# Optimization experiments

Measured on AMD Instinct MI355X. Metric: run time of the kernel, lower is better.

The kernel has to match this reference:

```python
import jax, jax.numpy as jnp
import numpy as np

S, B, D, H, L = 512, 512, 300, 256, 3

def setup_inputs() -> dict:
    key = jax.random.key(0)
    ks = jax.random.split(key, 9)
    sc = 0.02
    return {
        "x": jax.random.normal(ks[0], (S, B, D), dtype=jnp.float32),
        "fW_ih0": jax.random.normal(ks[1], (D, H), dtype=jnp.float32) * sc,
        "fW_ih": jax.random.normal(ks[2], (L - 1, H, H), dtype=jnp.float32) * sc,
        "fW_hh": jax.random.normal(ks[3], (L, H, H), dtype=jnp.float32) * sc,
        "fb": jnp.zeros((L, H), dtype=jnp.float32),
        "bW_ih0": jax.random.normal(ks[4], (D, H), dtype=jnp.float32) * sc,
        "bW_ih": jax.random.normal(ks[5], (L - 1, H, H), dtype=jnp.float32) * sc,
        "bW_hh": jax.random.normal(ks[6], (L, H, H), dtype=jnp.float32) * sc,
        "bb": jnp.zeros((L, H), dtype=jnp.float32),
    }

def _run_rnn(x, W_ih0, W_ih, W_hh, b):
    # x: [S, B, D]; stacked vanilla tanh RNN with L layers.
    batch = x.shape[1]
    h0 = jnp.zeros((L, batch, H), dtype=x.dtype)

    def step(h, x_t):  # h: [L, B, H], x_t: [B, D]
        inp = x_t
        new_h = []
        for l in range(L):
            Wih = W_ih0 if l == 0 else W_ih[l - 1]
            hl = jnp.tanh(inp @ Wih + h[l] @ W_hh[l] + b[l])
            new_h.append(hl)
            inp = hl
        return jnp.stack(new_h, axis=0), None

    h_final, _ = jax.lax.scan(step, h0, x)
    return h_final  # [L, B, H]

def reference(x, fW_ih0, fW_ih, fW_hh, fb, bW_ih0, bW_ih, bW_hh, bb):
    hf = _run_rnn(x, fW_ih0, fW_ih, fW_hh, fb)          # forward direction
    hb = _run_rnn(x[::-1], bW_ih0, bW_ih, bW_hh, bb)    # backward direction
    return jnp.concatenate((hf[-1], hb[-1]), axis=-1)   # [B, 2H]
```

## Files before the change

### kernel.cpp

```cpp
#include <hip/hip_runtime.h>
#include <cstdint>
#include <cstddef>


#define SEQ   512
#define BATCH 512
#define DIN   300
#define HDIM  256
#define NT    512
#define CH    64
#define NCH   (SEQ / CH)
#define NSLOT (NCH + 2)
#define TS    16
#define ZTILE 131072

typedef _Float16 f16x8 __attribute__((ext_vector_type(8)));
typedef __fp16   fp16x2 __attribute__((ext_vector_type(2)));
typedef float    f32x4 __attribute__((ext_vector_type(4)));

#define WIH0_E 0
#define WHH_E  163840
#define WIHN_E 557056
#define HC_BYTE   1638400
#define HB_BYTE   3211264
#define Z0_BYTE   (HB_BYTE + 67108864)
#define Z1_BYTE   (Z0_BYTE + 268435456)
#define Z2_BYTE   (Z1_BYTE + 67108864)
#define RING_E    8388608ull

static __device__ __forceinline__ uint16_t f16bits(_Float16 h) {
    union { _Float16 h; uint16_t u; } v; v.h = h; return v.u;
}
static __device__ __forceinline__ uint32_t pk2(float a, float b) {
    union { fp16x2 h; uint32_t u; } v; v.h = __builtin_amdgcn_cvt_pkrtz(a, b); return v.u;
}
static __device__ __forceinline__ int swz(int row, int col) {
    return (row * 256 + col) ^ ((row & 7) << 3);
}

static __device__ __forceinline__ void aload8(f16x8 r[8], const _Float16* p, size_t stepE) {
    const _Float16* p0 = p;
    const _Float16* p1 = p + stepE;
    const _Float16* p2 = p + 2 * stepE;
    const _Float16* p3 = p + 3 * stepE;
    const _Float16* p4 = p + 4 * stepE;
    const _Float16* p5 = p + 5 * stepE;
    const _Float16* p6 = p + 6 * stepE;
    const _Float16* p7 = p + 7 * stepE;
    asm volatile(
        "global_load_dwordx4 %0, %8, off\n\t"
        "global_load_dwordx4 %1, %9, off\n\t"
        "global_load_dwordx4 %2, %10, off\n\t"
        "global_load_dwordx4 %3, %11, off\n\t"
        "global_load_dwordx4 %4, %12, off\n\t"
        "global_load_dwordx4 %5, %13, off\n\t"
        "global_load_dwordx4 %6, %14, off\n\t"
        "global_load_dwordx4 %7, %15, off\n\t"
        "s_waitcnt vmcnt(0)"
        : "=&v"(r[0]), "=&v"(r[1]), "=&v"(r[2]), "=&v"(r[3]),
          "=&v"(r[4]), "=&v"(r[5]), "=&v"(r[6]), "=&v"(r[7])
        : "v"(p0), "v"(p1), "v"(p2), "v"(p3), "v"(p4), "v"(p5), "v"(p6), "v"(p7)
        : "memory");
}

__global__ void rnn_prep(const float* __restrict__ fW_ih0, const float* __restrict__ fW_ih,
                         const float* __restrict__ fW_hh,  const float* __restrict__ bW_ih0,
                         const float* __restrict__ bW_ih,  const float* __restrict__ bW_hh,
                         _Float16* __restrict__ wf)
{
    const int gid = blockIdx.x * 256 + threadIdx.x;
    const int d = gid / 51200;
    const int r = gid - d * 51200;
    const int lane = r & 63;
    const float* Wih0 = d ? bW_ih0 : fW_ih0;
    const float* Wih  = d ? bW_ih  : fW_ih;
    const float* Whh  = d ? bW_hh  : fW_hh;
    _Float16 vals[8];
    size_t dstE;
    if (r < 10240) {
        const int ck = r >> 6, ct = ck / 10, kt = ck - ct * 10;
        const int col = ct * 16 + (lane & 15);
        const int k0  = kt * 32 + (lane >> 4) * 8;
        #pragma unroll
        for (int e = 0; e < 8; ++e) {
            const int k = k0 + e;
            vals[e] = (k < 300) ? (_Float16)Wih0[(size_t)k * 256 + col] : (_Float16)0.f;
        }
        dstE = (size_t)WIH0_E + (size_t)d * 81920 + (size_t)r * 8;
    } else if (r < 34816) {
        const int rr = r - 10240, l = rr / 8192, r2 = rr - l * 8192;
        const int ck = r2 >> 6, ct = ck >> 3, kt = ck & 7;
        const int col = ct * 16 + (lane & 15);
        const int k0  = kt * 32 + (lane >> 4) * 8;
        #pragma unroll
        for (int e = 0; e < 8; ++e)
            vals[e] = (_Float16)Whh[((size_t)(l * 256 + k0 + e)) * 256 + col];
        dstE = (size_t)WHH_E + (size_t)(d * 3 + l) * 65536 + (size_t)r2 * 8;
    } else {
        const int rr = r - 34816, ln = rr / 8192, r2 = rr - ln * 8192;
        const int ck = r2 >> 6, ct = ck >> 3, kt = ck & 7;
        const int col = ct * 16 + (lane & 15);
        const int k0  = kt * 32 + (lane >> 4) * 8;
        #pragma unroll
        for (int e = 0; e < 8; ++e)
            vals[e] = (_Float16)Wih[((size_t)(ln * 256 + k0 + e)) * 256 + col];
        dstE = (size_t)WIHN_E + (size_t)(d * 2 + ln) * 65536 + (size_t)r2 * 8;
    }
    *(f16x8*)(wf + dstE) = *(const f16x8*)vals;
}

__global__ __attribute__((amdgpu_flat_work_group_size(NT, NT)))
void rnn_gemm0(const float* __restrict__ x, const _Float16* __restrict__ wih0,
               const float* __restrict__ fb, const float* __restrict__ bb,
               uint16_t* __restrict__ z0)
{
    __shared__ uint16_t Xl[2][16 * 332];
    const int tid = threadIdx.x, lane = tid & 63, w = tid >> 6;
    const int colw = lane & 15, rq = lane >> 4, rq8 = rq * 8;
    const int ct0 = w * 2;
    const int sg = blockIdx.x >> 5, rb = blockIdx.x & 31;
    const int b0 = rb * 16;
    const size_t chunk = ((size_t)(rb * 8 + w) * 64 + lane) * 8;

    int rs[5], cc2[5]; bool pv[5];
    #pragma unroll
    for (int b = 0; b < 5; ++b) {
        const int p = tid + b * NT;
        pv[b] = p < 2400;
        const int r = p / 150;
        rs[b] = r; cc2[b] = (p - r * 150) * 2;
    }

    float bv[2][2];
    #pragma unroll
    for (int dd = 0; dd < 2; ++dd)
        #pragma unroll
        for (int c = 0; c < 2; ++c)
            bv[dd][c] = (dd ? bb : fb)[(ct0 + c) * 16 + colw];

    for (int p = tid; p < 320; p += NT) {
        const int bu = p / 160, q = p - bu * 160;
        const int r = q / 10, cc = 300 + (q - r * 10) * 2;
        *(uint32_t*)&Xl[bu][r * 332 + cc] = 0;
    }
    {
        const float* xs = x + ((size_t)(sg * TS) * BATCH + b0) * DIN;
        #pragma unroll
        for (int b = 0; b < 5; ++b) if (pv[b]) {
            const float2 v = *(const float2*)(xs + (size_t)rs[b] * DIN + cc2[b]);
            *(uint32_t*)&Xl[0][rs[b] * 332 + cc2[b]] = pk2(v.x, v.y);
        }
    }
    __syncthreads();

    #pragma unroll 1
    for (int si = 0; si < TS; ++si) {
        const int s = sg * TS + si;
        const int buf = si & 1;
        const bool last = (si == TS - 1);

        {
            f32x4 a0 = (f32x4){bv[0][0], bv[0][0], bv[0][0], bv[0][0]};
            f32x4 a1 = (f32x4){bv[0][1], bv[0][1], bv[0][1], bv[0][1]};
            #pragma unroll
            for (int kt = 0; kt < 10; ++kt) {
                const f16x8 wv0 = *(const f16x8*)(wih0 + (((size_t)ct0 * 10 + kt) * 64 + lane) * 8);
                const f16x8 wv1 = *(const f16x8*)(wih0 + (((size_t)(ct0 + 1) * 10 + kt) * 64 + lane) * 8);
                const f16x8 a = *(const f16x8*)&Xl[buf][colw * 332 + kt * 32 + rq8];
                a0 = __builtin_amdgcn_mfma_f32_16x16x32_f16(a, wv0, a0, 0, 0, 0);
                a1 = __builtin_amdgcn_mfma_f32_16x16x32_f16(a, wv1, a1, 0, 0, 0);
            }
            uint4 sv;
            sv.x = pk2(a0[0], a0[1]); sv.y = pk2(a0[2], a0[3]);
            sv.z = pk2(a1[0], a1[1]); sv.w = pk2(a1[2], a1[3]);
            *(uint4*)(z0 + (size_t)s * ZTILE + chunk) = sv;
        }

        float2 xr[5];
        if (!last) {
            const float* xs = x + ((size_t)(s + 1) * BATCH + b0) * DIN;
            #pragma unroll
            for (int b = 0; b < 5; ++b) if (pv[b])
                xr[b] = *(const float2*)(xs + (size_t)rs[b] * DIN + cc2[b]);
        }

        f32x4 a0 = (f32x4){bv[1][0], bv[1][0], bv[1][0], bv[1][0]};
        f32x4 a1 = (f32x4){bv[1][1], bv[1][1], bv[1][1], bv[1][1]};
        #pragma unroll
        for (int kt = 0; kt < 10; ++kt) {
            const f16x8 wv0 = *(const f16x8*)(wih0 + 81920 + (((size_t)ct0 * 10 + kt) * 64 + lane) * 8);
            const f16x8 wv1 = *(const f16x8*)(wih0 + 81920 + (((size_t)(ct0 + 1) * 10 + kt) * 64 + lane) * 8);
            const f16x8 a = *(const f16x8*)&Xl[buf][colw * 332 + kt * 32 + rq8];
            a0 = __builtin_amdgcn_mfma_f32_16x16x32_f16(a, wv0, a0, 0, 0, 0);
            a1 = __builtin_amdgcn_mfma_f32_16x16x32_f16(a, wv1, a1, 0, 0, 0);
        }

        if (!last) {
            #pragma unroll
            for (int b = 0; b < 5; ++b) if (pv[b])
                *(uint32_t*)&Xl[buf ^ 1][rs[b] * 332 + cc2[b]] = pk2(xr[b].x, xr[b].y);
        }

        {
            uint4 sv;
            sv.x = pk2(a0[0], a0[1]); sv.y = pk2(a0[2], a0[3]);
            sv.z = pk2(a1[0], a1[1]); sv.w = pk2(a1[2], a1[3]);
            *(uint4*)(z0 + ((size_t)SEQ + (SEQ - 1 - s)) * ZTILE + chunk) = sv;
        }

        __builtin_amdgcn_sched_barrier(0);
        asm volatile("s_waitcnt lgkmcnt(0)" ::: "memory");
        __builtin_amdgcn_s_barrier();
        __builtin_amdgcn_sched_barrier(0);
    }
}

template<int L>
__device__ __forceinline__ void rec_run(const _Float16* whh_all, const _Float16* wihn_all,
                                        const uint16_t* zsrc, uint16_t* zdst,
                                        uint16_t* hcarry, const float* fb, const float* bb,
                                        float* out, int d, int i, int cs, uint16_t* Hb)
{
    const int tid = threadIdx.x, lane = tid & 63, w = tid >> 6;
    const int colw = lane & 15, rq = lane >> 4, rq8 = rq * 8;
    const int ct0 = w * 2;
    const int grow0 = i * 16;

    const _Float16* whh = whh_all + (size_t)(d * 3 + L) * 65536;
    f16x8 wh0[8], wh1[8];
    aload8(wh0, whh + ((size_t)ct0 * 8 * 64 + lane) * 8, 512);
    aload8(wh1, whh + ((size_t)(ct0 + 1) * 8 * 64 + lane) * 8, 512);
    f16x8 wn0[8], wn1[8];
    float bn0 = 0.f, bn1 = 0.f;
    if constexpr (L < 2) {
        const _Float16* wnx = wihn_all + (size_t)(d * 2 + L) * 65536;
        aload8(wn0, wnx + ((size_t)ct0 * 8 * 64 + lane) * 8, 512);
        aload8(wn1, wnx + ((size_t)(ct0 + 1) * 8 * 64 + lane) * 8, 512);
        const float* bnx = (d ? bb : fb) + (L + 1) * HDIM;
        bn0 = bnx[ct0 * 16 + colw];
        bn1 = bnx[(ct0 + 1) * 16 + colw];
    }

    for (int p = tid; p < 4096; p += NT) ((uint32_t*)Hb)[p] = 0;
    __syncthreads();
    if (cs > 0) {
        const uint16_t* hc = hcarry + (size_t)(d * 3 + L) * 131072;
        const int row = tid >> 5, c8 = (tid & 31) * 8;
        *(uint4*)&Hb[4096 + ((row * 256 + c8) ^ ((row & 7) << 3))] =
            *(const uint4*)(hc + (size_t)(grow0 + row) * 256 + c8);
    }
    __syncthreads();

    const size_t zoff = ((size_t)(i * 8 + w) * 64 + lane) * 8;

    uint4 zc = *(const uint4*)(zsrc + zoff);
    uint4 za = *(const uint4*)(zsrc + (size_t)ZTILE + zoff);
    uint4 zb = *(const uint4*)(zsrc + 2 * (size_t)ZTILE + zoff);

    f32x4 anp0 = {}, anp1 = {};

    #pragma unroll 1
    for (int k = 0; k < CH; ++k) {
        const int cur = k & 1, prv = cur ^ 1;
        const int kp = (k + 3 < CH) ? (k + 3) : (CH - 1);
        const uint4 zd = *(const uint4*)(zsrc + (size_t)kp * ZTILE + zoff);

        f16x8 ah[8];
        #pragma unroll
        for (int kt = 0; kt < 8; ++kt)
            ah[kt] = *(const f16x8*)&Hb[(prv << 12) + swz(colw, kt * 32 + rq8)];

        f32x4 ar0, ar1;
        {
            union { uint4 u; _Float16 h[8]; } zz; zz.u = zc;
            ar0 = (f32x4){(float)zz.h[0], (float)zz.h[1], (float)zz.h[2], (float)zz.h[3]};
            ar1 = (f32x4){(float)zz.h[4], (float)zz.h[5], (float)zz.h[6], (float)zz.h[7]};
        }

        f32x4 an0, an1;
        if constexpr (L < 2) {
            an0 = (f32x4){bn0, bn0, bn0, bn0};
            an1 = (f32x4){bn1, bn1, bn1, bn1};
            #pragma unroll
            for (int kt = 0; kt < 8; ++kt) {
                ar0 = __builtin_amdgcn_mfma_f32_16x16x32_f16(ah[kt], wh0[kt], ar0, 0, 0, 0);
                ar1 = __builtin_amdgcn_mfma_f32_16x16x32_f16(ah[kt], wh1[kt], ar1, 0, 0, 0);
                an0 = __builtin_amdgcn_mfma_f32_16x16x32_f16(ah[kt], wn0[kt], an0, 0, 0, 0);
                an1 = __builtin_amdgcn_mfma_f32_16x16x32_f16(ah[kt], wn1[kt], an1, 0, 0, 0);
            }
        } else {
            f32x4 arB0 = {}, arB1 = {};
            #pragma unroll
            for (int kt = 0; kt < 4; ++kt) {
                ar0  = __builtin_amdgcn_mfma_f32_16x16x32_f16(ah[kt],     wh0[kt],     ar0,  0, 0, 0);
                ar1  = __builtin_amdgcn_mfma_f32_16x16x32_f16(ah[kt],     wh1[kt],     ar1,  0, 0, 0);
                arB0 = __builtin_amdgcn_mfma_f32_16x16x32_f16(ah[4 + kt], wh0[4 + kt], arB0, 0, 0, 0);
                arB1 = __builtin_amdgcn_mfma_f32_16x16x32_f16(ah[4 + kt], wh1[4 + kt], arB1, 0, 0, 0);
            }
            ar0 = ar0 + arB0;
            ar1 = ar1 + arB1;
        }

        if constexpr (L < 2) {
            if (k >= 2) {
                uint4 sv;
                sv.x = pk2(anp0[0], anp0[1]); sv.y = pk2(anp0[2], anp0[3]);
                sv.z = pk2(anp1[0], anp1[1]); sv.w = pk2(anp1[2], anp1[3]);
                *(uint4*)(zdst + (size_t)(k - 2) * ZTILE + zoff) = sv;
            }
        }

        float hv[8];
        #pragma unroll
        for (int q = 0; q < 8; ++q) {
            const float S = (q < 4) ? ar0[q] : ar1[q - 4];
            const float e = __builtin_amdgcn_exp2f(S * 2.885390081777927f);
            const float r = __builtin_amdgcn_rcpf(e + 1.f);
            hv[q] = __builtin_fmaf(-2.f, r, 1.f);
        }
        #pragma unroll
        for (int q = 0; q < 8; ++q) {
            const int c = q >> 2, j = q & 3;
            Hb[(cur << 12) + swz(rq * 4 + j, (ct0 + c) * 16 + colw)] = f16bits((_Float16)hv[q]);
        }
        if (L == 2 && cs == NCH - 1 && k == CH - 1) {
            #pragma unroll
            for (int q = 0; q < 8; ++q) {
                const int c = q >> 2, j = q & 3;
                out[(size_t)(grow0 + rq * 4 + j) * 512 + d * 256 + (ct0 + c) * 16 + colw] = hv[q];
            }
        }

        if constexpr (L < 2) { anp0 = an0; anp1 = an1; }
        zc = za; za = zb; zb = zd;

        __builtin_amdgcn_sched_barrier(0);
        asm volatile("s_waitcnt lgkmcnt(0)" ::: "memory");
        __builtin_amdgcn_s_barrier();
        __builtin_amdgcn_sched_barrier(0);
    }

    if constexpr (L < 2) {
        {
            uint4 sv;
            sv.x = pk2(anp0[0], anp0[1]); sv.y = pk2(anp0[2], anp0[3]);
            sv.z = pk2(anp1[0], anp1[1]); sv.w = pk2(anp1[2], anp1[3]);
            *(uint4*)(zdst + (size_t)(CH - 2) * ZTILE + zoff) = sv;
        }
        f32x4 an0 = (f32x4){bn0, bn0, bn0, bn0};
        f32x4 an1 = (f32x4){bn1, bn1, bn1, bn1};
        #pragma unroll
        for (int kt = 0; kt < 8; ++kt) {
            const f16x8 ah = *(const f16x8*)&Hb[(1 << 12) + swz(colw, kt * 32 + rq8)];
            an0 = __builtin_amdgcn_mfma_f32_16x16x32_f16(ah, wn0[kt], an0, 0, 0, 0);
            an1 = __builtin_amdgcn_mfma_f32_16x16x32_f16(ah, wn1[kt], an1, 0, 0, 0);
        }
        uint4 sv;
        sv.x = pk2(an0[0], an0[1]); sv.y = pk2(an0[2], an0[3]);
        sv.z = pk2(an1[0], an1[1]); sv.w = pk2(an1[2], an1[3]);
        *(uint4*)(zdst + (size_t)(CH - 1) * ZTILE + zoff) = sv;
    }
    {
        uint16_t* hc = hcarry + (size_t)(d * 3 + L) * 131072;
        const int row = tid >> 5, c8 = (tid & 31) * 8;
        *(uint4*)(hc + (size_t)(grow0 + row) * 256 + c8) =
            *(const uint4*)&Hb[4096 + ((row * 256 + c8) ^ ((row & 7) << 3))];
    }
}

__global__ __attribute__((amdgpu_flat_work_group_size(NT, NT), amdgpu_waves_per_eu(2)))
void rnn_rec(const _Float16* whh_all, const _Float16* wihn_all,
             uint16_t* z0, uint16_t* z1, uint16_t* z2,
             uint16_t* hcarry, const float* fb, const float* bb,
             float* out, int slot)
{
    __shared__ uint16_t Hb[2 * 4096];
    const int l = blockIdx.x >> 6, sub = blockIdx.x & 63;
    const int d = sub >> 5, i = sub & 31;
    const int cs = slot - l;
    if (cs < 0 || cs >= NCH) return;
    const size_t ringE = (size_t)((cs & 1) * 2 + d) * RING_E;
    if (l == 0) {
        const uint16_t* zs = z0 + ((size_t)d * SEQ + (size_t)cs * CH) * ZTILE;
        rec_run<0>(whh_all, wihn_all, zs, z1 + ringE, hcarry, fb, bb, out, d, i, cs, Hb);
    } else if (l == 1) {
        rec_run<1>(whh_all, wihn_all, z1 + ringE, z2 + ringE, hcarry, fb, bb, out, d, i, cs, Hb);
    } else {
        rec_run<2>(whh_all, wihn_all, z2 + ringE, nullptr, hcarry, fb, bb, out, d, i, cs, Hb);
    }
}

extern "C" void kernel_launch(void* const* d_in, const int* in_sizes, int n_in,
                              void* d_out, int out_size, void* d_ws, size_t ws_size,
                              hipStream_t stream)
{
    (void)in_sizes; (void)n_in; (void)out_size; (void)ws_size;
    const float* x      = (const float*)d_in[0];
    const float* fW_ih0 = (const float*)d_in[1];
    const float* fW_ih  = (const float*)d_in[2];
    const float* fW_hh  = (const float*)d_in[3];
    const float* fb     = (const float*)d_in[4];
    const float* bW_ih0 = (const float*)d_in[5];
    const float* bW_ih  = (const float*)d_in[6];
    const float* bW_hh  = (const float*)d_in[7];
    const float* bb     = (const float*)d_in[8];
    uint8_t* ws = (uint8_t*)d_ws;

    _Float16* wf     = (_Float16*)ws;
    uint16_t* hcarry = (uint16_t*)(ws + HC_BYTE);
    uint16_t* z0     = (uint16_t*)(ws + Z0_BYTE);
    uint16_t* z1     = (uint16_t*)(ws + Z1_BYTE);
    uint16_t* z2     = (uint16_t*)(ws + Z2_BYTE);
    const _Float16* whh  = wf + WHH_E;
    const _Float16* wihn = wf + WIHN_E;
    float* out = (float*)d_out;

    rnn_prep<<<400, 256, 0, stream>>>(fW_ih0, fW_ih, fW_hh, bW_ih0, bW_ih, bW_hh, wf);
    rnn_gemm0<<<1024, NT, 0, stream>>>(x, wf, fb, bb, z0);
    for (int s = 0; s < NSLOT; ++s)
        rnn_rec<<<192, NT, 0, stream>>>(whh, wihn, z0, z1, z2, hcarry, fb, bb, out, s);
}
```

Before: 872.9 us.

## Fuse input GEMM into slot kernel and overlap with recurrence chunks

The standalone input-projection GEMM is removed. Each slot launch now runs, next to the recurrent blocks, 128 extra blocks that compute the layer-0 input projections for the following chunk, so that GEMM overlaps the latency-bound recurrence. The recurrent loop is unrolled by four with a four-deep register prefetch ring for z, and the layer-0 MFMA chains are split into two accumulators. Weight loads no longer wait inside the asm helper; a separate drain waits for them. This adds one launch, shares LDS between the two roles, and raises register pressure.

Result: slower. 991.4 us (+13.6%).

```diff
diff --git a/kernel.cpp b/kernel.cpp
--- a/kernel.cpp
+++ b/kernel.cpp
@@ -10,9 +10,9 @@
 #define NT    512
 #define CH    64
 #define NCH   (SEQ / CH)
-#define NSLOT (NCH + 2)
 #define TS    16
 #define ZTILE 131072
+#define XLBUF 5312
 
 typedef _Float16 f16x8 __attribute__((ext_vector_type(8)));
 typedef __fp16   fp16x2 __attribute__((ext_vector_type(2)));
@@ -55,12 +55,15 @@
         "global_load_dwordx4 %4, %12, off\n\t"
         "global_load_dwordx4 %5, %13, off\n\t"
         "global_load_dwordx4 %6, %14, off\n\t"
-        "global_load_dwordx4 %7, %15, off\n\t"
-        "s_waitcnt vmcnt(0)"
+        "global_load_dwordx4 %7, %15, off"
         : "=&v"(r[0]), "=&v"(r[1]), "=&v"(r[2]), "=&v"(r[3]),
           "=&v"(r[4]), "=&v"(r[5]), "=&v"(r[6]), "=&v"(r[7])
         : "v"(p0), "v"(p1), "v"(p2), "v"(p3), "v"(p4), "v"(p5), "v"(p6), "v"(p7)
         : "memory");
+}
+static __device__ __forceinline__ void adrain() {
+    asm volatile("s_waitcnt vmcnt(0)" ::: "memory");
+    __builtin_amdgcn_sched_barrier(0);
 }
 
 __global__ void rnn_prep(const float* __restrict__ fW_ih0, const float* __restrict__ fW_ih,
@@ -109,18 +112,20 @@
     *(f16x8*)(wf + dstE) = *(const f16x8*)vals;
 }
 
-__global__ __attribute__((amdgpu_flat_work_group_size(NT, NT)))
-void rnn_gemm0(const float* __restrict__ x, const _Float16* __restrict__ wih0,
-               const float* __restrict__ fb, const float* __restrict__ bb,
-               uint16_t* __restrict__ z0)
+__device__ __forceinline__ void gemm0_chunk(const float* __restrict__ x,
+                                            const _Float16* __restrict__ wih0,
+                                            const float* __restrict__ fb,
+                                            const float* __restrict__ bb,
+                                            uint16_t* __restrict__ z0,
+                                            int chunk, int gb, uint16_t* Xl)
 {
-    __shared__ uint16_t Xl[2][16 * 332];
     const int tid = threadIdx.x, lane = tid & 63, w = tid >> 6;
     const int colw = lane & 15, rq = lane >> 4, rq8 = rq * 8;
     const int ct0 = w * 2;
-    const int sg = blockIdx.x >> 5, rb = blockIdx.x & 31;
+    const int sg4 = gb >> 5, rb = gb & 31;
     const int b0 = rb * 16;
-    const size_t chunk = ((size_t)(rb * 8 + w) * 64 + lane) * 8;
+    const int sbase = chunk * CH + sg4 * TS;
+    const size_t chunkoff = ((size_t)(rb * 8 + w) * 64 + lane) * 8;
 
     int rs[5], cc2[5]; bool pv[5];
     #pragma unroll
@@ -141,21 +146,21 @@
     for (int p = tid; p < 320; p += NT) {
         const int bu = p / 160, q = p - bu * 160;
         const int r = q / 10, cc = 300 + (q - r * 10) * 2;
-        *(uint32_t*)&Xl[bu][r * 332 + cc] = 0;
+        *(uint32_t*)&Xl[bu * XLBUF + r * 332 + cc] = 0;
     }
     {
-        const float* xs = x + ((size_t)(sg * TS) * BATCH + b0) * DIN;
+        const float* xs = x + ((size_t)sbase * BATCH + b0) * DIN;
         #pragma unroll
         for (int b = 0; b < 5; ++b) if (pv[b]) {
             const float2 v = *(const float2*)(xs + (size_t)rs[b] * DIN + cc2[b]);
-            *(uint32_t*)&Xl[0][rs[b] * 332 + cc2[b]] = pk2(v.x, v.y);
+            *(uint32_t*)&Xl[rs[b] * 332 + cc2[b]] = pk2(v.x, v.y);
         }
     }
     __syncthreads();
 
     #pragma unroll 1
     for (int si = 0; si < TS; ++si) {
-        const int s = sg * TS + si;
+        const int s = sbase + si;
         const int buf = si & 1;
         const bool last = (si == TS - 1);
 
@@ -166,14 +171,14 @@
             for (int kt = 0; kt < 10; ++kt) {
                 const f16x8 wv0 = *(const f16x8*)(wih0 + (((size_t)ct0 * 10 + kt) * 64 + lane) * 8);
                 const f16x8 wv1 = *(const f16x8*)(wih0 + (((size_t)(ct0 + 1) * 10 + kt) * 64 + lane) * 8);
-                const f16x8 a = *(const f16x8*)&Xl[buf][colw * 332 + kt * 32 + rq8];
+                const f16x8 a = *(const f16x8*)&Xl[buf * XLBUF + colw * 332 + kt * 32 + rq8];
                 a0 = __builtin_amdgcn_mfma_f32_16x16x32_f16(a, wv0, a0, 0, 0, 0);
                 a1 = __builtin_amdgcn_mfma_f32_16x16x32_f16(a, wv1, a1, 0, 0, 0);
             }
             uint4 sv;
             sv.x = pk2(a0[0], a0[1]); sv.y = pk2(a0[2], a0[3]);
             sv.z = pk2(a1[0], a1[1]); sv.w = pk2(a1[2], a1[3]);
-            *(uint4*)(z0 + (size_t)s * ZTILE + chunk) = sv;
+            *(uint4*)(z0 + (size_t)s * ZTILE + chunkoff) = sv;
         }
 
         float2 xr[5];
@@ -184,28 +189,27 @@
                 xr[b] = *(const float2*)(xs + (size_t)rs[b] * DIN + cc2[b]);
         }
 
-        f32x4 a0 = (f32x4){bv[1][0], bv[1][0], bv[1][0], bv[1][0]};
-        f32x4 a1 = (f32x4){bv[1][1], bv[1][1], bv[1][1], bv[1][1]};
-        #pragma unroll
-        for (int kt = 0; kt < 10; ++kt) {
-            const f16x8 wv0 = *(const f16x8*)(wih0 + 81920 + (((size_t)ct0 * 10 + kt) * 64 + lane) * 8);
-            const f16x8 wv1 = *(const f16x8*)(wih0 + 81920 + (((size_t)(ct0 + 1) * 10 + kt) * 64 + lane) * 8);
-            const f16x8 a = *(const f16x8*)&Xl[buf][colw * 332 + kt * 32 + rq8];
-            a0 = __builtin_amdgcn_mfma_f32_16x16x32_f16(a, wv0, a0, 0, 0, 0);
-            a1 = __builtin_amdgcn_mfma_f32_16x16x32_f16(a, wv1, a1, 0, 0, 0);
-        }
-
-        if (!last) {
-            #pragma unroll
-            for (int b = 0; b < 5; ++b) if (pv[b])
-                *(uint32_t*)&Xl[buf ^ 1][rs[b] * 332 + cc2[b]] = pk2(xr[b].x, xr[b].y);
-        }
-
         {
+            f32x4 a0 = (f32x4){bv[1][0], bv[1][0], bv[1][0], bv[1][0]};
+            f32x4 a1 = (f32x4){bv[1][1], bv[1][1], bv[1][1], bv[1][1]};
+            #pragma unroll
+            for (int kt = 0; kt < 10; ++kt) {
+                const f16x8 wv0 = *(const f16x8*)(wih0 + 81920 + (((size_t)ct0 * 10 + kt) * 64 + lane) * 8);
+                const f16x8 wv1 = *(const f16x8*)(wih0 + 81920 + (((size_t)(ct0 + 1) * 10 + kt) * 64 + lane) * 8);
+                const f16x8 a = *(const f16x8*)&Xl[buf * XLBUF + colw * 332 + kt * 32 + rq8];
+                a0 = __builtin_amdgcn_mfma_f32_16x16x32_f16(a, wv0, a0, 0, 0, 0);
+                a1 = __builtin_amdgcn_mfma_f32_16x16x32_f16(a, wv1, a1, 0, 0, 0);
+            }
             uint4 sv;
             sv.x = pk2(a0[0], a0[1]); sv.y = pk2(a0[2], a0[3]);
             sv.z = pk2(a1[0], a1[1]); sv.w = pk2(a1[2], a1[3]);
-            *(uint4*)(z0 + ((size_t)SEQ + (SEQ - 1 - s)) * ZTILE + chunk) = sv;
+            *(uint4*)(z0 + ((size_t)SEQ + (SEQ - 1 - s)) * ZTILE + chunkoff) = sv;
+        }
+
+        if (!last) {
+            #pragma unroll
+            for (int b = 0; b < 5; ++b) if (pv[b])
+                *(uint32_t*)&Xl[(buf ^ 1) * XLBUF + rs[b] * 332 + cc2[b]] = pk2(xr[b].x, xr[b].y);
         }
 
         __builtin_amdgcn_sched_barrier(0);
@@ -240,6 +244,7 @@
         bn0 = bnx[ct0 * 16 + colw];
         bn1 = bnx[(ct0 + 1) * 16 + colw];
     }
+    adrain();
 
     for (int p = tid; p < 4096; p += NT) ((uint32_t*)Hb)[p] = 0;
     __syncthreads();
@@ -253,91 +258,105 @@
 
     const size_t zoff = ((size_t)(i * 8 + w) * 64 + lane) * 8;
 
-    uint4 zc = *(const uint4*)(zsrc + zoff);
-    uint4 za = *(const uint4*)(zsrc + (size_t)ZTILE + zoff);
-    uint4 zb = *(const uint4*)(zsrc + 2 * (size_t)ZTILE + zoff);
+    uint4 zp[4];
+    #pragma unroll
+    for (int j = 0; j < 4; ++j)
+        zp[j] = *(const uint4*)(zsrc + (size_t)j * ZTILE + zoff);
 
     f32x4 anp0 = {}, anp1 = {};
 
     #pragma unroll 1
-    for (int k = 0; k < CH; ++k) {
-        const int cur = k & 1, prv = cur ^ 1;
-        const int kp = (k + 3 < CH) ? (k + 3) : (CH - 1);
-        const uint4 zd = *(const uint4*)(zsrc + (size_t)kp * ZTILE + zoff);
-
-        f16x8 ah[8];
-        #pragma unroll
-        for (int kt = 0; kt < 8; ++kt)
-            ah[kt] = *(const f16x8*)&Hb[(prv << 12) + swz(colw, kt * 32 + rq8)];
-
-        f32x4 ar0, ar1;
-        {
-            union { uint4 u; _Float16 h[8]; } zz; zz.u = zc;
-            ar0 = (f32x4){(float)zz.h[0], (float)zz.h[1], (float)zz.h[2], (float)zz.h[3]};
-            ar1 = (f32x4){(float)zz.h[4], (float)zz.h[5], (float)zz.h[6], (float)zz.h[7]};
-        }
-
-        f32x4 an0, an1;
-        if constexpr (L < 2) {
-            an0 = (f32x4){bn0, bn0, bn0, bn0};
-            an1 = (f32x4){bn1, bn1, bn1, bn1};
-            #pragma unroll
-            for (int kt = 0; kt < 8; ++kt) {
-                ar0 = __builtin_amdgcn_mfma_f32_16x16x32_f16(ah[kt], wh0[kt], ar0, 0, 0, 0);
-                ar1 = __builtin_amdgcn_mfma_f32_16x16x32_f16(ah[kt], wh1[kt], ar1, 0, 0, 0);
-                an0 = __builtin_amdgcn_mfma_f32_16x16x32_f16(ah[kt], wn0[kt], an0, 0, 0, 0);
-                an1 = __builtin_amdgcn_mfma_f32_16x16x32_f16(ah[kt], wn1[kt], an1, 0, 0, 0);
-            }
-        } else {
-            f32x4 arB0 = {}, arB1 = {};
-            #pragma unroll
-            for (int kt = 0; kt < 4; ++kt) {
-                ar0  = __builtin_amdgcn_mfma_f32_16x16x32_f16(ah[kt],     wh0[kt],     ar0,  0, 0, 0);
-                ar1  = __builtin_amdgcn_mfma_f32_16x16x32_f16(ah[kt],     wh1[kt],     ar1,  0, 0, 0);
-                arB0 = __builtin_amdgcn_mfma_f32_16x16x32_f16(ah[4 + kt], wh0[4 + kt], arB0, 0, 0, 0);
-                arB1 = __builtin_amdgcn_mfma_f32_16x16x32_f16(ah[4 + kt], wh1[4 + kt], arB1, 0, 0, 0);
-            }
-            ar0 = ar0 + arB0;
-            ar1 = ar1 + arB1;
-        }
-
-        if constexpr (L < 2) {
-            if (k >= 2) {
-                uint4 sv;
-                sv.x = pk2(anp0[0], anp0[1]); sv.y = pk2(anp0[2], anp0[3]);
-                sv.z = pk2(anp1[0], anp1[1]); sv.w = pk2(anp1[2], anp1[3]);
-                *(uint4*)(zdst + (size_t)(k - 2) * ZTILE + zoff) = sv;
-            }
-        }
-
-        float hv[8];
-        #pragma unroll
-        for (int q = 0; q < 8; ++q) {
-            const float S = (q < 4) ? ar0[q] : ar1[q - 4];
-            const float e = __builtin_amdgcn_exp2f(S * 2.885390081777927f);
-            const float r = __builtin_amdgcn_rcpf(e + 1.f);
-            hv[q] = __builtin_fmaf(-2.f, r, 1.f);
-        }
-        #pragma unroll
-        for (int q = 0; q < 8; ++q) {
-            const int c = q >> 2, j = q & 3;
-            Hb[(cur << 12) + swz(rq * 4 + j, (ct0 + c) * 16 + colw)] = f16bits((_Float16)hv[q]);
-        }
-        if (L == 2 && cs == NCH - 1 && k == CH - 1) {
+    for (int k0 = 0; k0 < CH; k0 += 4) {
+        #pragma unroll
+        for (int u = 0; u < 4; ++u) {
+            const int k = k0 + u;
+            const int cur = u & 1, prv = cur ^ 1;
+
+            f32x4 ar0a, ar1a;
+            {
+                union { uint4 v; _Float16 h[8]; } zz; zz.v = zp[u];
+                ar0a = (f32x4){(float)zz.h[0], (float)zz.h[1], (float)zz.h[2], (float)zz.h[3]};
+                ar1a = (f32x4){(float)zz.h[4], (float)zz.h[5], (float)zz.h[6], (float)zz.h[7]};
+            }
+            {
+                const int kp = (k + 4 < CH) ? (k + 4) : (CH - 1);
+                zp[u] = *(const uint4*)(zsrc + (size_t)kp * ZTILE + zoff);
+            }
+
+            f16x8 ah[8];
+            #pragma unroll
+            for (int kt = 0; kt < 8; ++kt)
+                ah[kt] = *(const f16x8*)&Hb[(prv << 12) + swz(colw, kt * 32 + rq8)];
+
+            f32x4 ar0, ar1, an0, an1;
+            if constexpr (L < 2) {
+                f32x4 ar0b = {}, ar1b = {};
+                f32x4 an0a = (f32x4){bn0, bn0, bn0, bn0}, an0b = {};
+                f32x4 an1a = (f32x4){bn1, bn1, bn1, bn1}, an1b = {};
+                #pragma unroll
+                for (int kt = 0; kt < 4; ++kt) {
+                    ar0a = __builtin_amdgcn_mfma_f32_16x16x32_f16(ah[kt],     wh0[kt],     ar0a, 0, 0, 0);
+                    ar1a = __builtin_amdgcn_mfma_f32_16x16x32_f16(ah[kt],     wh1[kt],     ar1a, 0, 0, 0);
+                    an0a = __builtin_amdgcn_mfma_f32_16x16x32_f16(ah[kt],     wn0[kt],     an0a, 0, 0, 0);
+                    an1a = __builtin_amdgcn_mfma_f32_16x16x32_f16(ah[kt],     wn1[kt],     an1a, 0, 0, 0);
+                    ar0b = __builtin_amdgcn_mfma_f32_16x16x32_f16(ah[4 + kt], wh0[4 + kt], ar0b, 0, 0, 0);
+                    ar1b = __builtin_amdgcn_mfma_f32_16x16x32_f16(ah[4 + kt], wh1[4 + kt], ar1b, 0, 0, 0);
+                    an0b = __builtin_amdgcn_mfma_f32_16x16x32_f16(ah[4 + kt], wn0[4 + kt], an0b, 0, 0, 0);
+                    an1b = __builtin_amdgcn_mfma_f32_16x16x32_f16(ah[4 + kt], wn1[4 + kt], an1b, 0, 0, 0);
+                }
+                ar0 = ar0a + ar0b; ar1 = ar1a + ar1b;
+                an0 = an0a + an0b; an1 = an1a + an1b;
+            } else {
+                f32x4 arB0 = {}, arB1 = {};
+                #pragma unroll
+                for (int kt = 0; kt < 4; ++kt) {
+                    ar0a = __builtin_amdgcn_mfma_f32_16x16x32_f16(ah[kt],     wh0[kt],     ar0a, 0, 0, 0);
+                    ar1a = __builtin_amdgcn_mfma_f32_16x16x32_f16(ah[kt],     wh1[kt],     ar1a, 0, 0, 0);
+                    arB0 = __builtin_amdgcn_mfma_f32_16x16x32_f16(ah[4 + kt], wh0[4 + kt], arB0, 0, 0, 0);
+                    arB1 = __builtin_amdgcn_mfma_f32_16x16x32_f16(ah[4 + kt], wh1[4 + kt], arB1, 0, 0, 0);
+                }
+                ar0 = ar0a + arB0;
+                ar1 = ar1a + arB1;
+                an0 = an0; an1 = an1;
+            }
+
+            if constexpr (L < 2) {
+                if (k >= 2) {
+                    uint4 sv;
+                    sv.x = pk2(anp0[0], anp0[1]); sv.y = pk2(anp0[2], anp0[3]);
+                    sv.z = pk2(anp1[0], anp1[1]); sv.w = pk2(anp1[2], anp1[3]);
+                    *(uint4*)(zdst + (size_t)(k - 2) * ZTILE + zoff) = sv;
+                }
+            }
+
+            float hv[8];
+            #pragma unroll
+            for (int q = 0; q < 8; ++q) {
+                const float S = (q < 4) ? ar0[q] : ar1[q - 4];
+                const float e = __builtin_amdgcn_exp2f(S * 2.885390081777927f);
+                const float r = __builtin_amdgcn_rcpf(e + 1.f);
+                hv[q] = __builtin_fmaf(-2.f, r, 1.f);
+            }
             #pragma unroll
             for (int q = 0; q < 8; ++q) {
                 const int c = q >> 2, j = q & 3;
-                out[(size_t)(grow0 + rq * 4 + j) * 512 + d * 256 + (ct0 + c) * 16 + colw] = hv[q];
-            }
-        }
-
-        if constexpr (L < 2) { anp0 = an0; anp1 = an1; }
-        zc = za; za = zb; zb = zd;
-
-        __builtin_amdgcn_sched_barrier(0);
-        asm volatile("s_waitcnt lgkmcnt(0)" ::: "memory");
-        __builtin_amdgcn_s_barrier();
-        __builtin_amdgcn_sched_barrier(0);
+                Hb[(cur << 12) + swz(rq * 4 + j, (ct0 + c) * 16 + colw)] = f16bits((_Float16)hv[q]);
+            }
+            if (L == 2 && cs == NCH - 1 && k == CH - 1) {
+                #pragma unroll
+                for (int q = 0; q < 8; ++q) {
+                    const int c = q >> 2, j = q & 3;
+                    out[(size_t)(grow0 + rq * 4 + j) * 512 + d * 256 + (ct0 + c) * 16 + colw] = hv[q];
+                }
+            }
+
+            if constexpr (L < 2) { anp0 = an0; anp1 = an1; }
+
+            __builtin_amdgcn_sched_barrier(0);
+            asm volatile("s_waitcnt lgkmcnt(0)" ::: "memory");
+            __builtin_amdgcn_s_barrier();
+            __builtin_amdgcn_sched_barrier(0);
+        }
     }
 
     if constexpr (L < 2) {
@@ -369,24 +388,31 @@
 }
 
 __global__ __attribute__((amdgpu_flat_work_group_size(NT, NT), amdgpu_waves_per_eu(2)))
-void rnn_rec(const _Float16* whh_all, const _Float16* wihn_all,
-             uint16_t* z0, uint16_t* z1, uint16_t* z2,
-             uint16_t* hcarry, const float* fb, const float* bb,
-             float* out, int slot)
+void rnn_slot(const float* x, const _Float16* wf0,
+              const _Float16* whh_all, const _Float16* wihn_all,
+              uint16_t* z0, uint16_t* z1, uint16_t* z2,
+              uint16_t* hcarry, const float* fb, const float* bb,
+              float* out, int slot)
 {
-    __shared__ uint16_t Hb[2 * 4096];
-    const int l = blockIdx.x >> 6, sub = blockIdx.x & 63;
-    const int d = sub >> 5, i = sub & 31;
-    const int cs = slot - l;
-    if (cs < 0 || cs >= NCH) return;
-    const size_t ringE = (size_t)((cs & 1) * 2 + d) * RING_E;
-    if (l == 0) {
-        const uint16_t* zs = z0 + ((size_t)d * SEQ + (size_t)cs * CH) * ZTILE;
-        rec_run<0>(whh_all, wihn_all, zs, z1 + ringE, hcarry, fb, bb, out, d, i, cs, Hb);
-    } else if (l == 1) {
-        rec_run<1>(whh_all, wihn_all, z1 + ringE, z2 + ringE, hcarry, fb, bb, out, d, i, cs, Hb);
+    __shared__ uint16_t SH[2 * XLBUF];
+    if (blockIdx.x < 192) {
+        const int l = blockIdx.x >> 6, sub = blockIdx.x & 63;
+        const int d = sub >> 5, i = sub & 31;
+        const int cs = slot - l;
+        if (cs < 0 || cs >= NCH) return;
+        const size_t ringE = (size_t)((cs & 1) * 2 + d) * RING_E;
+        if (l == 0) {
+            const uint16_t* zs = z0 + ((size_t)d * SEQ + (size_t)cs * CH) * ZTILE;
+            rec_run<0>(whh_all, wihn_all, zs, z1 + ringE, hcarry, fb, bb, out, d, i, cs, SH);
+        } else if (l == 1) {
+            rec_run<1>(whh_all, wihn_all, z1 + ringE, z2 + ringE, hcarry, fb, bb, out, d, i, cs, SH);
+        } else {
+            rec_run<2>(whh_all, wihn_all, z2 + ringE, nullptr, hcarry, fb, bb, out, d, i, cs, SH);
+        }
     } else {
-        rec_run<2>(whh_all, wihn_all, z2 + ringE, nullptr, hcarry, fb, bb, out, d, i, cs, Hb);
+        const int chunk = slot + 1;
+        if (chunk < 0 || chunk >= NCH) return;
+        gemm0_chunk(x, wf0, fb, bb, z0, chunk, blockIdx.x - 192, SH);
     }
 }
 
@@ -416,7 +442,6 @@
     float* out = (float*)d_out;
 
     rnn_prep<<<400, 256, 0, stream>>>(fW_ih0, fW_ih, fW_hh, bW_ih0, bW_ih, bW_hh, wf);
-    rnn_gemm0<<<1024, NT, 0, stream>>>(x, wf, fb, bb, z0);
-    for (int s = 0; s < NSLOT; ++s)
-        rnn_rec<<<192, NT, 0, stream>>>(whh, wihn, z0, z1, z2, hcarry, fb, bb, out, s);
-}
+    for (int s = -1; s <= 9; ++s)
+        rnn_slot<<<320, NT, 0, stream>>>(x, wf, whh, wihn, z0, z1, z2, hcarry, fb, bb, out, s);
+}
```
